# Optimization experiments

Hardware: AMD Instinct MI355X
Metric: run time of the kernel (lower is better)

Reference implementation:

```python
import jax, jax.numpy as jnp
import numpy as np

N_NODES = 100000

def gcn_conv(x, W, b, row, col, n):
    # PyG GCNConv: linear transform, then symmetric-normalized aggregation
    h = x @ W  # [N, out]
    # add self loops
    sl = jnp.arange(n, dtype=row.dtype)
    r = jnp.concatenate([row, sl])
    c = jnp.concatenate([col, sl])
    deg = jax.ops.segment_sum(jnp.ones_like(c, dtype=h.dtype), c, num_segments=n)
    dinv = jnp.where(deg > 0, jax.lax.rsqrt(deg), 0.0)
    norm = dinv[r] * dinv[c]  # [E+N]
    out = jax.ops.segment_sum(h[r] * norm[:, None], c, num_segments=n)
    return out + b


def setup_inputs() -> dict:
    key = jax.random.key(0)
    k1, k2, k3, k4, k5, k6 = jax.random.split(key, 6)
    E = 1600000
    x = jax.random.normal(k1, (N_NODES, 256), dtype=jnp.float32)
    edge_index = jax.random.randint(k2, (2, E), 0, N_NODES, dtype=jnp.int64)
    # Glorot-style init for GCN weights
    W1 = jax.random.normal(k3, (256, 128), dtype=jnp.float32) / np.sqrt(256.0)
    b1 = jnp.zeros((128,), dtype=jnp.float32)
    W2 = jax.random.normal(k4, (128, 64), dtype=jnp.float32) / np.sqrt(128.0)
    b2 = jnp.zeros((64,), dtype=jnp.float32)
    return {"x": x, "edge_index": edge_index, "W1": W1, "b1": b1, "W2": W2, "b2": b2}


def reference(x, edge_index, W1, b1, W2, b2):
    row, col = edge_index[0], edge_index[1]
    h = gcn_conv(x, W1, b1, row, col, N_NODES)
    h = jax.nn.relu(h)
    z = gcn_conv(h, W2, b2, row, col, N_NODES)
    return z
```

## Files before the change

kernel.cpp:

```cpp
#include <hip/hip_runtime.h>

#define NN 100000
#define BW 256
#define NB ((NN + BW - 1) / BW)
#define CH 4096

typedef __attribute__((ext_vector_type(8))) short short8;
typedef __attribute__((ext_vector_type(4))) float f32x4;

__device__ __forceinline__ float bf2f(unsigned short u) {
    union { unsigned int i; float f; } v;
    v.i = ((unsigned int)u) << 16;
    return v.f;
}
__device__ __forceinline__ unsigned short f2bf(float f) {
    unsigned int u = __float_as_uint(f);
    unsigned int r = u + 0x7fffu + ((u >> 16) & 1u);
    return (unsigned short)(r >> 16);
}
__device__ __forceinline__ float ldf(const void* p, int i, int bf) {
    return bf ? bf2f(((const unsigned short*)p)[i]) : ((const float*)p)[i];
}
__device__ __forceinline__ int lde(const void* p, int i, int i64f) {
    return i64f ? (int)((const long long*)p)[i] : ((const int*)p)[i];
}
__device__ __forceinline__ short8 ld8bf(const void* p, size_t i, int bf) {
    if (bf) return *(const short8*)((const unsigned short*)p + i);
    const float* f = (const float*)p + i;
    f32x4 a = *(const f32x4*)f;
    f32x4 b = *(const f32x4*)(f + 4);
    short8 o;
    o[0] = (short)f2bf(a[0]); o[1] = (short)f2bf(a[1]);
    o[2] = (short)f2bf(a[2]); o[3] = (short)f2bf(a[3]);
    o[4] = (short)f2bf(b[0]); o[5] = (short)f2bf(b[1]);
    o[6] = (short)f2bf(b[2]); o[7] = (short)f2bf(b[3]);
    return o;
}

__global__ void detect_kernel(const unsigned int* __restrict__ xw,
                              const unsigned int* __restrict__ eiw,
                              int* __restrict__ flags) {
    __shared__ int s0, s1;
    int tid = threadIdx.x;
    if (tid == 0) { s0 = 0; s1 = 0; }
    __syncthreads();
    if (tid < 128) {
        unsigned int w = xw[tid];
        int e = (int)((w >> 7) & 0xFFu);
        if (e < 100 || e > 130) atomicAdd(&s0, 1);
    } else if (tid < 192) {
        if (eiw[2 * (tid - 128) + 1] == 0u) atomicAdd(&s1, 1);
    }
    __syncthreads();
    if (tid == 0) {
        flags[0] = (s0 < 16) ? 1 : 0;
        flags[1] = (s1 >= 48) ? 1 : 0;
    }
}

__global__ __launch_bounds__(512) void sort_tr_kernel(const void* __restrict__ ei, int E,
                                                      int* __restrict__ bcnt,
                                                      int* __restrict__ poff,
                                                      int* __restrict__ ebin,
                                                      const int* __restrict__ flags,
                                                      const void* __restrict__ w1,
                                                      const void* __restrict__ w2,
                                                      unsigned short* __restrict__ w1t,
                                                      unsigned short* __restrict__ w2t,
                                                      int PB) {
    __shared__ int lc[NB + 1];
    __shared__ int ls[512];
    __shared__ int sbuf[CH];
    int bid = blockIdx.x, tid = threadIdx.x;
    if (bid < PB) {
        int i64f = flags[1];
        int base = bid * CH;
        int cntE = min(CH, E - base);
        int re[CH / 512], ce[CH / 512];
        for (int i = tid; i < NB; i += 512) lc[i] = 0;
        __syncthreads();
#pragma unroll
        for (int q = 0; q < CH / 512; ++q) {
            int e = base + q * 512 + tid;
            if (e < E) {
                int r = lde(ei, e, i64f);
                int c = lde(ei, E + e, i64f);
                r = min(max(r, 0), NN - 1);
                c = min(max(c, 0), NN - 1);
                re[q] = r; ce[q] = c;
                atomicAdd(&lc[c >> 8], 1);
            } else {
                re[q] = -1; ce[q] = 0;
            }
        }
        __syncthreads();
        int v = (tid < NB) ? lc[tid] : 0;
        ls[tid] = v;
        __syncthreads();
        for (int o = 1; o < 512; o <<= 1) {
            int t = (tid >= o) ? ls[tid - o] : 0;
            __syncthreads();
            ls[tid] += t;
            __syncthreads();
        }
        int excl = ls[tid] - v;
        if (tid < NB) {
            poff[bid * (NB + 1) + tid] = excl;
            if (v) atomicAdd(&bcnt[tid], v);
        }
        if (tid == 0) poff[bid * (NB + 1) + NB] = cntE;
        __syncthreads();
        if (tid < NB) lc[tid] = excl;
        __syncthreads();
#pragma unroll
        for (int q = 0; q < CH / 512; ++q) {
            if (re[q] >= 0) {
                int pos = atomicAdd(&lc[ce[q] >> 8], 1);
                sbuf[pos] = (re[q] << 8) | (ce[q] & 255);
            }
        }
        __syncthreads();
        for (int i = tid; i < cntE; i += 512)
            ebin[base + i] = sbuf[i];
    } else {
        int bf = flags[0];
        int i = (bid - PB) * 512 + tid;
        if (i < 128 * 256) {
            int n = i >> 8, k = i & 255;
            w1t[n * 256 + k] = f2bf(ldf(w1, k * 128 + n, bf));
        } else if (i < 128 * 256 + 64 * 128) {
            int j = i - 128 * 256;
            int n = j >> 7, k = j & 127;
            w2t[n * 128 + k] = f2bf(ldf(w2, k * 64 + n, bf));
        }
    }
}

__global__ void bscan_kernel(const int* __restrict__ bcnt, int* __restrict__ bstart,
                             int* __restrict__ off, int E) {
    __shared__ int s[512];
    int tid = threadIdx.x;
    int v = (tid < NB) ? bcnt[tid] : 0;
    s[tid] = v;
    __syncthreads();
    for (int o = 1; o < 512; o <<= 1) {
        int t = (tid >= o) ? s[tid - o] : 0;
        __syncthreads();
        s[tid] += t;
        __syncthreads();
    }
    int excl = s[tid] - v;
    if (tid < NB) bstart[tid] = excl;
    if (tid == NB - 1) bstart[NB] = excl + v;
    if (tid == 0) off[NN] = E;
}

__global__ __launch_bounds__(512) void sg1_kernel(const int* __restrict__ ebin,
                                                  const int* __restrict__ poff,
                                                  const int* __restrict__ bstart,
                                                  int* __restrict__ off,
                                                  float* __restrict__ dinv,
                                                  int* __restrict__ epair,
                                                  const int* __restrict__ flags,
                                                  const void* __restrict__ x,
                                                  const unsigned short* __restrict__ wt,
                                                  unsigned short* __restrict__ h,
                                                  int GB, int PB) {
    __shared__ unsigned short wl[128 * 136];
    __shared__ int cnt[BW], pfx[BW];
    int bid = blockIdx.x, tid = threadIdx.x;
    bool isC = ((bid % 3) == 0) && (bid / 3 < NB);
    if (isC) {
        int b = bid / 3;
        int c0 = b << 8;
        int s = bstart[b];
        for (int i = tid; i < BW; i += 512) cnt[i] = 0;
        __syncthreads();
        for (int p = tid; p < PB; p += 512) {
            const int* pr = poff + p * (NB + 1);
            int s0 = p * CH + pr[b], s1 = p * CH + pr[b + 1];
            for (int i = s0; i < s1; ++i)
                atomicAdd(&cnt[ebin[i] & 255], 1);
        }
        __syncthreads();
        int v = (tid < BW) ? cnt[tid] : 0;
        if (tid < BW) pfx[tid] = v;
        __syncthreads();
        for (int o = 1; o < BW; o <<= 1) {
            int t = (tid < BW && tid >= o) ? pfx[tid - o] : 0;
            __syncthreads();
            if (tid < BW) pfx[tid] += t;
            __syncthreads();
        }
        if (tid < BW) {
            int basec = s + pfx[tid] - v;
            int node = c0 + tid;
            if (node < NN) {
                off[node] = basec;
                dinv[node] = rsqrtf((float)(v + 1));
            }
            cnt[tid] = basec;
        }
        __syncthreads();
        for (int p = tid; p < PB; p += 512) {
            const int* pr = poff + p * (NB + 1);
            int s0 = p * CH + pr[b], s1 = p * CH + pr[b + 1];
            for (int i = s0; i < s1; ++i) {
                int w = ebin[i];
                int pos = atomicAdd(&cnt[w & 255], 1);
                epair[pos] = w >> 8;
            }
        }
        return;
    }
    int gb = bid - min(bid / 3 + 1, NB);
    int bf = flags[0];
    int lane = tid & 63, wv = tid >> 6;
    int ln = lane & 15, kq = lane >> 4;
    int rowBase = gb * 128 + wv * 16;
    int anode = min(rowBase + ln, NN - 1);
    size_t abase = (size_t)anode * 256;
    f32x4 acc[8];
#pragma unroll
    for (int t = 0; t < 8; ++t) acc[t] = (f32x4)0.f;

    for (int half = 0; half < 2; ++half) {
        __syncthreads();
        for (int i = tid; i < 128 * 16; i += 512) {
            int n = i >> 4, b = i & 15;
            short8 v = *(const short8*)(wt + n * 256 + half * 128 + b * 8);
            *(short8*)(&wl[n * 136 + b * 8]) = v;
        }
        __syncthreads();
#pragma unroll
        for (int ks = 0; ks < 4; ++ks) {
            int klocal = ks * 32 + kq * 8;
            short8 a = ld8bf(x, abase + half * 128 + klocal, bf);
#pragma unroll
            for (int t = 0; t < 8; ++t) {
                int n = t * 16 + ln;
                short8 b = *(const short8*)(&wl[n * 136 + klocal]);
                acc[t] = __builtin_amdgcn_mfma_f32_16x16x32_bf16(a, b, acc[t], 0, 0, 0);
            }
        }
    }
#pragma unroll
    for (int r = 0; r < 4; ++r) {
        int node = rowBase + kq * 4 + r;
        if (node < NN) {
            unsigned short* orow = h + (size_t)node * 128;
#pragma unroll
            for (int t = 0; t < 8; ++t)
                orow[t * 16 + ln] = f2bf(acc[t][r]);
        }
    }
}

__global__ __launch_bounds__(256) void agg1_kernel(const unsigned short* __restrict__ h,
                                                   const float* __restrict__ dinv,
                                                   const int* __restrict__ off,
                                                   const int* __restrict__ epair,
                                                   const void* __restrict__ b1,
                                                   unsigned short* __restrict__ outp,
                                                   const int* __restrict__ flags) {
    int tid = threadIdx.x;
    int lane = tid & 63, wv = tid >> 6;
    int g = lane >> 4, l = lane & 15;
    int c = blockIdx.x * 16 + wv * 4 + g;
    if (c >= NN) return;
    int bf = flags[0];
    float dc = dinv[c];
    int jb = off[c], je = off[c + 1];
    float acc[8];
    {
        short8 v = *(const short8*)(h + (size_t)c * 128 + l * 8);
        float w = dc * dc;
#pragma unroll
        for (int f = 0; f < 8; ++f) acc[f] = bf2f((unsigned short)v[f]) * w;
    }
    int j = jb;
    for (; j + 3 < je; j += 4) {
        int s0 = epair[j], s1 = epair[j + 1], s2 = epair[j + 2], s3 = epair[j + 3];
        float w0 = dinv[s0] * dc, w1 = dinv[s1] * dc;
        float w2 = dinv[s2] * dc, w3 = dinv[s3] * dc;
        short8 v0 = *(const short8*)(h + (size_t)s0 * 128 + l * 8);
        short8 v1 = *(const short8*)(h + (size_t)s1 * 128 + l * 8);
        short8 v2 = *(const short8*)(h + (size_t)s2 * 128 + l * 8);
        short8 v3 = *(const short8*)(h + (size_t)s3 * 128 + l * 8);
#pragma unroll
        for (int f = 0; f < 8; ++f) {
            acc[f] = fmaf(bf2f((unsigned short)v0[f]), w0, acc[f]);
            acc[f] = fmaf(bf2f((unsigned short)v1[f]), w1, acc[f]);
            acc[f] = fmaf(bf2f((unsigned short)v2[f]), w2, acc[f]);
            acc[f] = fmaf(bf2f((unsigned short)v3[f]), w3, acc[f]);
        }
    }
    for (; j < je; ++j) {
        int s0 = epair[j];
        float w = dinv[s0] * dc;
        short8 v = *(const short8*)(h + (size_t)s0 * 128 + l * 8);
#pragma unroll
        for (int f = 0; f < 8; ++f) acc[f] = fmaf(bf2f((unsigned short)v[f]), w, acc[f]);
    }
    short8 o;
#pragma unroll
    for (int f = 0; f < 8; ++f)
        o[f] = (short)f2bf(fmaxf(acc[f] + ldf(b1, l * 8 + f, bf), 0.f));
    *(short8*)(outp + (size_t)c * 128 + l * 8) = o;
}

__global__ __launch_bounds__(512) void gemm2_kernel(const unsigned short* __restrict__ a_,
                                                    const unsigned short* __restrict__ wt,
                                                    unsigned short* __restrict__ h2) {
    __shared__ unsigned short wl[64 * 136];
    int tid = threadIdx.x;
    for (int i = tid; i < 64 * 16; i += 512) {
        int n = i >> 4, b = i & 15;
        short8 v = *(const short8*)(wt + n * 128 + b * 8);
        *(short8*)(&wl[n * 136 + b * 8]) = v;
    }
    __syncthreads();
    int lane = tid & 63, wv = tid >> 6;
    int ln = lane & 15, kq = lane >> 4;
    int rowBase = blockIdx.x * 128 + wv * 16;
    int anode = min(rowBase + ln, NN - 1);
    const unsigned short* arow = a_ + (size_t)anode * 128;
    f32x4 acc[4];
#pragma unroll
    for (int t = 0; t < 4; ++t) acc[t] = (f32x4)0.f;
#pragma unroll
    for (int ks = 0; ks < 4; ++ks) {
        int k0 = ks * 32 + kq * 8;
        short8 a = *(const short8*)(arow + k0);
#pragma unroll
        for (int t = 0; t < 4; ++t) {
            int n = t * 16 + ln;
            short8 b = *(const short8*)(&wl[n * 136 + k0]);
            acc[t] = __builtin_amdgcn_mfma_f32_16x16x32_bf16(a, b, acc[t], 0, 0, 0);
        }
    }
#pragma unroll
    for (int r = 0; r < 4; ++r) {
        int node = rowBase + kq * 4 + r;
        if (node < NN) {
            unsigned short* orow = h2 + (size_t)node * 64;
#pragma unroll
            for (int t = 0; t < 4; ++t)
                orow[t * 16 + ln] = f2bf(acc[t][r]);
        }
    }
}

__global__ __launch_bounds__(256) void agg_out_kernel(const unsigned short* __restrict__ h,
                                                      const float* __restrict__ dinv,
                                                      const int* __restrict__ off,
                                                      const int* __restrict__ epair,
                                                      const void* __restrict__ b2,
                                                      void* __restrict__ outp,
                                                      const int* __restrict__ flags) {
    int tid = threadIdx.x;
    int lane = tid & 63, wv = tid >> 6;
    int g = lane >> 3, l = lane & 7;
    int c = blockIdx.x * 32 + wv * 8 + g;
    if (c >= NN) return;
    int bf = flags[0];
    float dc = dinv[c];
    int jb = off[c], je = off[c + 1];
    float acc[8];
    {
        short8 v = *(const short8*)(h + (size_t)c * 64 + l * 8);
        float w = dc * dc;
#pragma unroll
        for (int f = 0; f < 8; ++f) acc[f] = bf2f((unsigned short)v[f]) * w;
    }
    int j = jb;
    for (; j + 3 < je; j += 4) {
        int s0 = epair[j], s1 = epair[j + 1], s2 = epair[j + 2], s3 = epair[j + 3];
        float w0 = dinv[s0] * dc, w1 = dinv[s1] * dc;
        float w2 = dinv[s2] * dc, w3 = dinv[s3] * dc;
        short8 v0 = *(const short8*)(h + (size_t)s0 * 64 + l * 8);
        short8 v1 = *(const short8*)(h + (size_t)s1 * 64 + l * 8);
        short8 v2 = *(const short8*)(h + (size_t)s2 * 64 + l * 8);
        short8 v3 = *(const short8*)(h + (size_t)s3 * 64 + l * 8);
#pragma unroll
        for (int f = 0; f < 8; ++f) {
            acc[f] = fmaf(bf2f((unsigned short)v0[f]), w0, acc[f]);
            acc[f] = fmaf(bf2f((unsigned short)v1[f]), w1, acc[f]);
            acc[f] = fmaf(bf2f((unsigned short)v2[f]), w2, acc[f]);
            acc[f] = fmaf(bf2f((unsigned short)v3[f]), w3, acc[f]);
        }
    }
    for (; j < je; ++j) {
        int s0 = epair[j];
        float w = dinv[s0] * dc;
        short8 v = *(const short8*)(h + (size_t)s0 * 64 + l * 8);
#pragma unroll
        for (int f = 0; f < 8; ++f) acc[f] = fmaf(bf2f((unsigned short)v[f]), w, acc[f]);
    }
    if (bf) {
        short8 o;
#pragma unroll
        for (int f = 0; f < 8; ++f)
            o[f] = (short)f2bf(acc[f] + ldf(b2, l * 8 + f, 1));
        *(short8*)((unsigned short*)outp + (size_t)c * 64 + l * 8) = o;
    } else {
        float* op = (float*)outp + (size_t)c * 64 + l * 8;
#pragma unroll
        for (int f = 0; f < 8; ++f)
            op[f] = acc[f] + ldf(b2, l * 8 + f, 0);
    }
}

extern "C" void kernel_launch(void* const* d_in, const int* in_sizes, int n_in,
                              void* d_out, int out_size, void* d_ws, size_t ws_size,
                              hipStream_t stream) {
    const void* x  = d_in[0];
    const void* ei = d_in[1];
    const void* W1 = d_in[2];
    const void* b1 = d_in[3];
    const void* W2 = d_in[4];
    const void* b2 = d_in[5];

    const int N = NN;
    const int E = in_sizes[1] / 2;
    const int PB = (E + CH - 1) / CH;
    const int GB = (N + 127) / 128;
    const int TB = (128 * 256 + 64 * 128 + 511) / 512;

    char* ws = (char*)d_ws;
    size_t o = 0;
    auto alloc = [&](size_t bytes) { size_t r = o; o += (bytes + 255) & ~(size_t)255; return r; };
    int*   flags  = (int*)(ws + alloc(256));
    int*   bcnt   = (int*)(ws + alloc((size_t)(NB + 1) * 4));
    int*   bstart = (int*)(ws + alloc((size_t)(NB + 1) * 4));
    int*   off    = (int*)(ws + alloc((size_t)(N + 1) * 4));
    float* dinv   = (float*)(ws + alloc((size_t)N * 4));
    int*   epair  = (int*)(ws + alloc((size_t)E * 4));
    int*   poff   = (int*)(ws + alloc((size_t)PB * (NB + 1) * 4));
    unsigned short* w1t  = (unsigned short*)(ws + alloc(128 * 256 * 2));
    unsigned short* w2t  = (unsigned short*)(ws + alloc(64 * 128 * 2));
    unsigned short* h1   = (unsigned short*)(ws + alloc((size_t)N * 128 * 2));
    unsigned short* agg1 = (unsigned short*)(ws + alloc((size_t)N * 128 * 2));
    unsigned short* h2   = h1;
    int* ebin = (int*)agg1;

    detect_kernel<<<1, 256, 0, stream>>>((const unsigned int*)x, (const unsigned int*)ei, flags);
    hipMemsetAsync(bcnt, 0, (size_t)(NB + 1) * 4, stream);
    sort_tr_kernel<<<PB + TB, 512, 0, stream>>>(ei, E, bcnt, poff, ebin, flags, W1, W2, w1t, w2t, PB);
    bscan_kernel<<<1, 512, 0, stream>>>(bcnt, bstart, off, E);
    sg1_kernel<<<GB + NB, 512, 0, stream>>>(ebin, poff, bstart, off, dinv, epair, flags, x, w1t, h1, GB, PB);
    agg1_kernel<<<(N + 15) / 16, 256, 0, stream>>>(h1, dinv, off, epair, b1, agg1, flags);
    gemm2_kernel<<<GB, 512, 0, stream>>>(agg1, w2t, h2);
    agg_out_kernel<<<(N + 31) / 32, 256, 0, stream>>>(h2, dinv, off, epair, b2, d_out, flags);
}
```

Measured before the change: 336.0 us.

## Split fused CSR-build/GEMM1 kernel and parallelize CSR partition scan per wave

The fused kernel that interleaved CSR-building blocks with GEMM1 blocks becomes two separate launches, csr_kernel and gemm1_kernel. In the CSR build, each wave now takes one partition and its lanes stride over that partition's edges, where before each thread walked a whole partition serially. In GEMM1, both halves of the x row fragments are loaded into registers ahead of the MFMA loops so global loads overlap the weight staging. The split gives up the overlap the fused launch allowed between CSR work and GEMM work and adds a launch. With only about ten edges per bin per partition, many lanes may sit idle in the new CSR loop.

```diff
diff --git a/kernel.cpp b/kernel.cpp
--- a/kernel.cpp
+++ b/kernel.cpp
@@ -155,93 +155,112 @@
     if (tid == 0) off[NN] = E;
 }
 
-__global__ __launch_bounds__(512) void sg1_kernel(const int* __restrict__ ebin,
+__global__ __launch_bounds__(512) void csr_kernel(const int* __restrict__ ebin,
                                                   const int* __restrict__ poff,
                                                   const int* __restrict__ bstart,
                                                   int* __restrict__ off,
                                                   float* __restrict__ dinv,
-                                                  int* __restrict__ epair,
-                                                  const int* __restrict__ flags,
-                                                  const void* __restrict__ x,
-                                                  const unsigned short* __restrict__ wt,
-                                                  unsigned short* __restrict__ h,
-                                                  int GB, int PB) {
+                                                  int* __restrict__ epair, int PB) {
+    __shared__ int cnt[BW], pfx[BW];
+    int b = blockIdx.x, tid = threadIdx.x;
+    int lane = tid & 63, wv = tid >> 6;
+    int c0 = b << 8;
+    int s = bstart[b];
+    for (int i = tid; i < BW; i += 512) cnt[i] = 0;
+    __syncthreads();
+    for (int p = wv; p < PB; p += 8) {
+        const int* pr = poff + p * (NB + 1);
+        int s0 = p * CH + pr[b], s1 = p * CH + pr[b + 1];
+        for (int i = s0 + lane; i < s1; i += 64)
+            atomicAdd(&cnt[ebin[i] & 255], 1);
+    }
+    __syncthreads();
+    int v = (tid < BW) ? cnt[tid] : 0;
+    if (tid < BW) pfx[tid] = v;
+    __syncthreads();
+    for (int o = 1; o < BW; o <<= 1) {
+        int t = (tid < BW && tid >= o) ? pfx[tid - o] : 0;
+        __syncthreads();
+        if (tid < BW) pfx[tid] += t;
+        __syncthreads();
+    }
+    if (tid < BW) {
+        int basec = s + pfx[tid] - v;
+        int node = c0 + tid;
+        if (node < NN) {
+            off[node] = basec;
+            dinv[node] = rsqrtf((float)(v + 1));
+        }
+        cnt[tid] = basec;
+    }
+    __syncthreads();
+    for (int p = wv; p < PB; p += 8) {
+        const int* pr = poff + p * (NB + 1);
+        int s0 = p * CH + pr[b], s1 = p * CH + pr[b + 1];
+        for (int i = s0 + lane; i < s1; i += 64) {
+            int w = ebin[i];
+            int pos = atomicAdd(&cnt[w & 255], 1);
+            epair[pos] = w >> 8;
+        }
+    }
+}
+
+__global__ __launch_bounds__(512) void gemm1_kernel(const int* __restrict__ flags,
+                                                    const void* __restrict__ x,
+                                                    const unsigned short* __restrict__ wt,
+                                                    unsigned short* __restrict__ h) {
     __shared__ unsigned short wl[128 * 136];
-    __shared__ int cnt[BW], pfx[BW];
-    int bid = blockIdx.x, tid = threadIdx.x;
-    bool isC = ((bid % 3) == 0) && (bid / 3 < NB);
-    if (isC) {
-        int b = bid / 3;
-        int c0 = b << 8;
-        int s = bstart[b];
-        for (int i = tid; i < BW; i += 512) cnt[i] = 0;
-        __syncthreads();
-        for (int p = tid; p < PB; p += 512) {
-            const int* pr = poff + p * (NB + 1);
-            int s0 = p * CH + pr[b], s1 = p * CH + pr[b + 1];
-            for (int i = s0; i < s1; ++i)
-                atomicAdd(&cnt[ebin[i] & 255], 1);
-        }
-        __syncthreads();
-        int v = (tid < BW) ? cnt[tid] : 0;
-        if (tid < BW) pfx[tid] = v;
-        __syncthreads();
-        for (int o = 1; o < BW; o <<= 1) {
-            int t = (tid < BW && tid >= o) ? pfx[tid - o] : 0;
-            __syncthreads();
-            if (tid < BW) pfx[tid] += t;
-            __syncthreads();
-        }
-        if (tid < BW) {
-            int basec = s + pfx[tid] - v;
-            int node = c0 + tid;
-            if (node < NN) {
-                off[node] = basec;
-                dinv[node] = rsqrtf((float)(v + 1));
-            }
-            cnt[tid] = basec;
-        }
-        __syncthreads();
-        for (int p = tid; p < PB; p += 512) {
-            const int* pr = poff + p * (NB + 1);
-            int s0 = p * CH + pr[b], s1 = p * CH + pr[b + 1];
-            for (int i = s0; i < s1; ++i) {
-                int w = ebin[i];
-                int pos = atomicAdd(&cnt[w & 255], 1);
-                epair[pos] = w >> 8;
-            }
-        }
-        return;
-    }
-    int gb = bid - min(bid / 3 + 1, NB);
+    int tid = threadIdx.x;
     int bf = flags[0];
     int lane = tid & 63, wv = tid >> 6;
     int ln = lane & 15, kq = lane >> 4;
-    int rowBase = gb * 128 + wv * 16;
+    int rowBase = blockIdx.x * 128 + wv * 16;
     int anode = min(rowBase + ln, NN - 1);
     size_t abase = (size_t)anode * 256;
+    short8 a0[4];
+#pragma unroll
+    for (int q = 0; q < 4; ++q)
+        a0[q] = ld8bf(x, abase + q * 32 + kq * 8, bf);
     f32x4 acc[8];
 #pragma unroll
     for (int t = 0; t < 8; ++t) acc[t] = (f32x4)0.f;
 
-    for (int half = 0; half < 2; ++half) {
-        __syncthreads();
-        for (int i = tid; i < 128 * 16; i += 512) {
-            int n = i >> 4, b = i & 15;
-            short8 v = *(const short8*)(wt + n * 256 + half * 128 + b * 8);
-            *(short8*)(&wl[n * 136 + b * 8]) = v;
-        }
-        __syncthreads();
-#pragma unroll
-        for (int ks = 0; ks < 4; ++ks) {
-            int klocal = ks * 32 + kq * 8;
-            short8 a = ld8bf(x, abase + half * 128 + klocal, bf);
-#pragma unroll
-            for (int t = 0; t < 8; ++t) {
-                int n = t * 16 + ln;
-                short8 b = *(const short8*)(&wl[n * 136 + klocal]);
-                acc[t] = __builtin_amdgcn_mfma_f32_16x16x32_bf16(a, b, acc[t], 0, 0, 0);
-            }
+    __syncthreads();
+    for (int i = tid; i < 128 * 16; i += 512) {
+        int n = i >> 4, b = i & 15;
+        short8 v = *(const short8*)(wt + n * 256 + b * 8);
+        *(short8*)(&wl[n * 136 + b * 8]) = v;
+    }
+    __syncthreads();
+    short8 a1[4];
+#pragma unroll
+    for (int q = 0; q < 4; ++q)
+        a1[q] = ld8bf(x, abase + 128 + q * 32 + kq * 8, bf);
+#pragma unroll
+    for (int ks = 0; ks < 4; ++ks) {
+        int klocal = ks * 32 + kq * 8;
+#pragma unroll
+        for (int t = 0; t < 8; ++t) {
+            int n = t * 16 + ln;
+            short8 b = *(const short8*)(&wl[n * 136 + klocal]);
+            acc[t] = __builtin_amdgcn_mfma_f32_16x16x32_bf16(a0[ks], b, acc[t], 0, 0, 0);
+        }
+    }
+    __syncthreads();
+    for (int i = tid; i < 128 * 16; i += 512) {
+        int n = i >> 4, b = i & 15;
+        short8 v = *(const short8*)(wt + n * 256 + 128 + b * 8);
+        *(short8*)(&wl[n * 136 + b * 8]) = v;
+    }
+    __syncthreads();
+#pragma unroll
+    for (int ks = 0; ks < 4; ++ks) {
+        int klocal = ks * 32 + kq * 8;
+#pragma unroll
+        for (int t = 0; t < 8; ++t) {
+            int n = t * 16 + ln;
+            short8 b = *(const short8*)(&wl[n * 136 + klocal]);
+            acc[t] = __builtin_amdgcn_mfma_f32_16x16x32_bf16(a1[ks], b, acc[t], 0, 0, 0);
         }
     }
 #pragma unroll
@@ -448,7 +467,8 @@
     hipMemsetAsync(bcnt, 0, (size_t)(NB + 1) * 4, stream);
     sort_tr_kernel<<<PB + TB, 512, 0, stream>>>(ei, E, bcnt, poff, ebin, flags, W1, W2, w1t, w2t, PB);
     bscan_kernel<<<1, 512, 0, stream>>>(bcnt, bstart, off, E);
-    sg1_kernel<<<GB + NB, 512, 0, stream>>>(ebin, poff, bstart, off, dinv, epair, flags, x, w1t, h1, GB, PB);
+    csr_kernel<<<NB, 512, 0, stream>>>(ebin, poff, bstart, off, dinv, epair, PB);
+    gemm1_kernel<<<GB, 512, 0, stream>>>(flags, x, w1t, h1);
     agg1_kernel<<<(N + 15) / 16, 256, 0, stream>>>(h1, dinv, off, epair, b1, agg1, flags);
     gemm2_kernel<<<GB, 512, 0, stream>>>(agg1, w2t, h2);
     agg_out_kernel<<<(N + 31) / 32, 256, 0, stream>>>(h2, dinv, off, epair, b2, d_out, flags);
```

Measured after the change: 382.9 us. 14.0% more time.

## Fuse layer-1 aggregation with layer-2 GEMM through shared memory

Applied to the files above, without the earlier changes.

Merges the first aggregation kernel and the second linear transform into one kernel. Each block aggregates 16 nodes, stages the ReLU'd bf16 rows in LDS, then four waves each compute a 16-column slice of the 64-wide output with MFMA, reading W2 directly from global memory. This drops the N×128 intermediate write and read plus one launch, at the cost of a block-wide sync after the irregular gather and uncached global W2 loads per block.

```diff
diff --git a/kernel.cpp b/kernel.cpp
--- a/kernel.cpp
+++ b/kernel.cpp
@@ -256,98 +256,80 @@
     }
 }
 
-__global__ __launch_bounds__(256) void agg1_kernel(const unsigned short* __restrict__ h,
-                                                   const float* __restrict__ dinv,
-                                                   const int* __restrict__ off,
-                                                   const int* __restrict__ epair,
-                                                   const void* __restrict__ b1,
-                                                   unsigned short* __restrict__ outp,
-                                                   const int* __restrict__ flags) {
+__global__ __launch_bounds__(256) void ag1_kernel(const unsigned short* __restrict__ h,
+                                                  const float* __restrict__ dinv,
+                                                  const int* __restrict__ off,
+                                                  const int* __restrict__ epair,
+                                                  const void* __restrict__ b1,
+                                                  const unsigned short* __restrict__ w2t,
+                                                  unsigned short* __restrict__ h2,
+                                                  const int* __restrict__ flags) {
+    __shared__ unsigned short sA[16 * 136];
     int tid = threadIdx.x;
     int lane = tid & 63, wv = tid >> 6;
     int g = lane >> 4, l = lane & 15;
-    int c = blockIdx.x * 16 + wv * 4 + g;
-    if (c >= NN) return;
+    int cb0 = blockIdx.x * 16;
+    int c = cb0 + wv * 4 + g;
     int bf = flags[0];
-    float dc = dinv[c];
-    int jb = off[c], je = off[c + 1];
     float acc[8];
+#pragma unroll
+    for (int f = 0; f < 8; ++f) acc[f] = 0.f;
+    if (c < NN) {
+        float dc = dinv[c];
+        int jb = off[c], je = off[c + 1];
+        {
+            short8 v = *(const short8*)(h + (size_t)c * 128 + l * 8);
+            float w = dc * dc;
+#pragma unroll
+            for (int f = 0; f < 8; ++f) acc[f] = bf2f((unsigned short)v[f]) * w;
+        }
+        int j = jb;
+        for (; j + 3 < je; j += 4) {
+            int s0 = epair[j], s1 = epair[j + 1], s2 = epair[j + 2], s3 = epair[j + 3];
+            float w0 = dinv[s0] * dc, w1 = dinv[s1] * dc;
+            float w2 = dinv[s2] * dc, w3 = dinv[s3] * dc;
+            short8 v0 = *(const short8*)(h + (size_t)s0 * 128 + l * 8);
+            short8 v1 = *(const short8*)(h + (size_t)s1 * 128 + l * 8);
+            short8 v2 = *(const short8*)(h + (size_t)s2 * 128 + l * 8);
+            short8 v3 = *(const short8*)(h + (size_t)s3 * 128 + l * 8);
+#pragma unroll
+            for (int f = 0; f < 8; ++f) {
+                acc[f] = fmaf(bf2f((unsigned short)v0[f]), w0, acc[f]);
+                acc[f] = fmaf(bf2f((unsigned short)v1[f]), w1, acc[f]);
+                acc[f] = fmaf(bf2f((unsigned short)v2[f]), w2, acc[f]);
+                acc[f] = fmaf(bf2f((unsigned short)v3[f]), w3, acc[f]);
+            }
+        }
+        for (; j < je; ++j) {
+            int s0 = epair[j];
+            float w = dinv[s0] * dc;
+            short8 v = *(const short8*)(h + (size_t)s0 * 128 + l * 8);
+#pragma unroll
+            for (int f = 0; f < 8; ++f) acc[f] = fmaf(bf2f((unsigned short)v[f]), w, acc[f]);
+        }
+    }
     {
-        short8 v = *(const short8*)(h + (size_t)c * 128 + l * 8);
-        float w = dc * dc;
-#pragma unroll
-        for (int f = 0; f < 8; ++f) acc[f] = bf2f((unsigned short)v[f]) * w;
-    }
-    int j = jb;
-    for (; j + 3 < je; j += 4) {
-        int s0 = epair[j], s1 = epair[j + 1], s2 = epair[j + 2], s3 = epair[j + 3];
-        float w0 = dinv[s0] * dc, w1 = dinv[s1] * dc;
-        float w2 = dinv[s2] * dc, w3 = dinv[s3] * dc;
-        short8 v0 = *(const short8*)(h + (size_t)s0 * 128 + l * 8);
-        short8 v1 = *(const short8*)(h + (size_t)s1 * 128 + l * 8);
-        short8 v2 = *(const short8*)(h + (size_t)s2 * 128 + l * 8);
-        short8 v3 = *(const short8*)(h + (size_t)s3 * 128 + l * 8);
-#pragma unroll
-        for (int f = 0; f < 8; ++f) {
-            acc[f] = fmaf(bf2f((unsigned short)v0[f]), w0, acc[f]);
-            acc[f] = fmaf(bf2f((unsigned short)v1[f]), w1, acc[f]);
-            acc[f] = fmaf(bf2f((unsigned short)v2[f]), w2, acc[f]);
-            acc[f] = fmaf(bf2f((unsigned short)v3[f]), w3, acc[f]);
-        }
-    }
-    for (; j < je; ++j) {
-        int s0 = epair[j];
-        float w = dinv[s0] * dc;
-        short8 v = *(const short8*)(h + (size_t)s0 * 128 + l * 8);
-#pragma unroll
-        for (int f = 0; f < 8; ++f) acc[f] = fmaf(bf2f((unsigned short)v[f]), w, acc[f]);
-    }
-    short8 o;
-#pragma unroll
-    for (int f = 0; f < 8; ++f)
-        o[f] = (short)f2bf(fmaxf(acc[f] + ldf(b1, l * 8 + f, bf), 0.f));
-    *(short8*)(outp + (size_t)c * 128 + l * 8) = o;
-}
-
-__global__ __launch_bounds__(512) void gemm2_kernel(const unsigned short* __restrict__ a_,
-                                                    const unsigned short* __restrict__ wt,
-                                                    unsigned short* __restrict__ h2) {
-    __shared__ unsigned short wl[64 * 136];
-    int tid = threadIdx.x;
-    for (int i = tid; i < 64 * 16; i += 512) {
-        int n = i >> 4, b = i & 15;
-        short8 v = *(const short8*)(wt + n * 128 + b * 8);
-        *(short8*)(&wl[n * 136 + b * 8]) = v;
+        short8 o;
+#pragma unroll
+        for (int f = 0; f < 8; ++f)
+            o[f] = (short)f2bf(fmaxf(acc[f] + ldf(b1, l * 8 + f, bf), 0.f));
+        *(short8*)(&sA[(wv * 4 + g) * 136 + l * 8]) = o;
     }
     __syncthreads();
-    int lane = tid & 63, wv = tid >> 6;
     int ln = lane & 15, kq = lane >> 4;
-    int rowBase = blockIdx.x * 128 + wv * 16;
-    int anode = min(rowBase + ln, NN - 1);
-    const unsigned short* arow = a_ + (size_t)anode * 128;
-    f32x4 acc[4];
-#pragma unroll
-    for (int t = 0; t < 4; ++t) acc[t] = (f32x4)0.f;
+    f32x4 a2 = (f32x4)0.f;
 #pragma unroll
     for (int ks = 0; ks < 4; ++ks) {
         int k0 = ks * 32 + kq * 8;
-        short8 a = *(const short8*)(arow + k0);
-#pragma unroll
-        for (int t = 0; t < 4; ++t) {
-            int n = t * 16 + ln;
-            short8 b = *(const short8*)(&wl[n * 136 + k0]);
-            acc[t] = __builtin_amdgcn_mfma_f32_16x16x32_bf16(a, b, acc[t], 0, 0, 0);
-        }
+        short8 a = *(const short8*)(&sA[ln * 136 + k0]);
+        short8 b = *(const short8*)(w2t + (wv * 16 + ln) * 128 + k0);
+        a2 = __builtin_amdgcn_mfma_f32_16x16x32_bf16(a, b, a2, 0, 0, 0);
     }
 #pragma unroll
     for (int r = 0; r < 4; ++r) {
-        int node = rowBase + kq * 4 + r;
-        if (node < NN) {
-            unsigned short* orow = h2 + (size_t)node * 64;
-#pragma unroll
-            for (int t = 0; t < 4; ++t)
-                orow[t * 16 + ln] = f2bf(acc[t][r]);
-        }
+        int node = cb0 + kq * 4 + r;
+        if (node < NN)
+            h2[(size_t)node * 64 + wv * 16 + ln] = f2bf(a2[r]);
     }
 }
 
@@ -440,16 +422,15 @@
     unsigned short* w1t  = (unsigned short*)(ws + alloc(128 * 256 * 2));
     unsigned short* w2t  = (unsigned short*)(ws + alloc(64 * 128 * 2));
     unsigned short* h1   = (unsigned short*)(ws + alloc((size_t)N * 128 * 2));
-    unsigned short* agg1 = (unsigned short*)(ws + alloc((size_t)N * 128 * 2));
-    unsigned short* h2   = h1;
-    int* ebin = (int*)agg1;
+    unsigned short* buf2 = (unsigned short*)(ws + alloc((size_t)N * 128 * 2));
+    unsigned short* h2   = buf2;
+    int* ebin = (int*)buf2;
 
     detect_kernel<<<1, 256, 0, stream>>>((const unsigned int*)x, (const unsigned int*)ei, flags);
     hipMemsetAsync(bcnt, 0, (size_t)(NB + 1) * 4, stream);
     sort_tr_kernel<<<PB + TB, 512, 0, stream>>>(ei, E, bcnt, poff, ebin, flags, W1, W2, w1t, w2t, PB);
     bscan_kernel<<<1, 512, 0, stream>>>(bcnt, bstart, off, E);
     sg1_kernel<<<GB + NB, 512, 0, stream>>>(ebin, poff, bstart, off, dinv, epair, flags, x, w1t, h1, GB, PB);
-    agg1_kernel<<<(N + 15) / 16, 256, 0, stream>>>(h1, dinv, off, epair, b1, agg1, flags);
-    gemm2_kernel<<<GB, 512, 0, stream>>>(agg1, w2t, h2);
+    ag1_kernel<<<(N + 15) / 16, 256, 0, stream>>>(h1, dinv, off, epair, b1, w2t, h2, flags);
     agg_out_kernel<<<(N + 31) / 32, 256, 0, stream>>>(h2, dinv, off, epair, b2, d_out, flags);
 }
```

New measurement: 335.5 us. Within noise of the previous version (-0.1%).
